# Optimization experiments

Measured on AMD Instinct MI355X. Metric: run time of the kernel, lower is better.

## Reference

```python
import jax, jax.numpy as jnp
import numpy as np

SIGMA = 1e-4          # flow-matching sigma (init kwarg)
OT_EPS = 0.01         # entropic regularization for the batched OT solve
OT_ITERS = 100        # Sinkhorn iterations


def _sinkhorn_log(M, eps, iters):
    """Log-domain Sinkhorn with uniform marginals. M: [B,N,N] cost (max-normalized).
    Returns log coupling log(pi): [B,N,N]. GPU-native batched replacement for the
    per-sample pot.emd network-simplex solve in the original."""
    B, N, _ = M.shape
    loga = -jnp.log(jnp.asarray(N, M.dtype))  # uniform marginal log prob
    f = jnp.zeros((B, N), M.dtype)
    g = jnp.zeros((B, N), M.dtype)

    def body(carry, _):
        f, g = carry
        g = eps * (loga - jax.scipy.special.logsumexp((f[:, :, None] - M) / eps, axis=1))
        f = eps * (loga - jax.scipy.special.logsumexp((g[:, None, :] - M) / eps, axis=2))
        return (f, g), None

    (f, g), _ = jax.lax.scan(body, (f, g), None, length=iters)
    return (f[:, :, None] + g[:, None, :] - M) / eps


def setup_inputs() -> dict:
    key = jax.random.key(0)
    ks = jax.random.split(key, 8)
    B, N, F, H = 512, 150, 3, 512
    x = jax.random.normal(ks[0], (B, N, F), jnp.float32)
    mask = jnp.ones((B, N, 1), jnp.float32)
    t = jax.random.uniform(ks[1], (B,), jnp.float32)
    x0_noise = jax.random.normal(ks[2], (B, N, F), jnp.float32)
    eps_noise = jax.random.normal(ks[3], (B, N, F), jnp.float32)
    W1 = 0.05 * jax.random.normal(ks[4], (F + 1, H), jnp.float32)
    b1 = jnp.zeros((H,), jnp.float32)
    W2 = 0.05 * jax.random.normal(ks[5], (H, F), jnp.float32)
    b2 = jnp.zeros((F,), jnp.float32)
    return {"x": x, "mask": mask, "t": t, "x0_noise": x0_noise,
            "eps_noise": eps_noise, "W1": W1, "b1": b1, "W2": W2, "b2": b2}


def reference(x, mask, t, x0_noise, eps_noise, W1, b1, W2, b2):
    B, N, F = x.shape
    x0, x1 = x0_noise, x                        # noise source / data target

    # squared pairwise distances, per-batch max-normalized (as in the torch code)
    M = jnp.sum((x0[:, :, None, :] - x1[:, None, :, :]) ** 2, axis=-1)  # [B,N,N]
    M = M / jnp.max(M, axis=(1, 2), keepdims=True)
    M = jax.lax.stop_gradient(M)                # original detaches M before emd

    logpi = _sinkhorn_log(M, OT_EPS, OT_ITERS)  # [B,N,N] log OT coupling

    # Sample N i.i.d. (i, j) pairs per batch from the flattened coupling.
    # Row marginal of pi is uniform -> i ~ Uniform(N), j ~ pi[i, :] / (1/N).
    key = jax.random.key(42)
    ki, kj = jax.random.split(key)
    i = jax.random.randint(ki, (B, N), 0, N)                       # [B,N]
    rows = jnp.take_along_axis(logpi, i[:, :, None], axis=1)       # [B,N,N]
    j = jax.random.categorical(kj, rows, axis=-1)                  # [B,N]

    x0s = jnp.take_along_axis(x0, i[:, :, None], axis=1)           # [B,N,F]
    x1s = jnp.take_along_axis(x1, j[:, :, None], axis=1)           # [B,N,F]
    mask_ot = jnp.take_along_axis(mask, j[:, :, None], axis=1)     # [B,N,1]

    tb = t[:, None, None]                                          # [B,1,1]
    mu_t = x0s * tb + x1s * (1.0 - tb)
    y = mu_t + SIGMA * eps_noise
    ut = (x0s - x1s) * mask_ot

    # stand-in flow network: per-particle MLP on [y, t]
    h = jnp.concatenate([y, jnp.broadcast_to(tb, (B, N, 1))], axis=-1)  # [B,N,F+1]
    h = jax.nn.gelu(h @ W1 + b1)
    vt = (h @ W2 + b2) * mask_ot

    return jnp.mean((vt - ut) ** 2)
```

## Files before the change

### kernel.cpp

```cpp
#include <hip/hip_runtime.h>
#include <cstdint>

#define B_ 512
#define N_ 150
#define NT 640
#define PPS 152
#define C1f 144.26950408889634f
#define LN2f 0.69314718055994531f
#define SIGMAf 1.0e-4f
#define INV_N (1.0f/150.0f)

#define EXP2R(x) __builtin_amdgcn_exp2f(x)
#define LOG2R(x) __builtin_amdgcn_logf(x)

#define DPPF(v, c) __int_as_float(__builtin_amdgcn_update_dpp( \
    __float_as_int(v), __float_as_int(v), (c), 0xF, 0xF, false))
#define RED4_ADD(v)  { v = v + DPPF(v, 0xB1); v = v + DPPF(v, 0x4E); }

#define REP10(X) X(0) X(1) X(2) X(3) X(4) X(5) X(6) X(7) X(8) X(9)

__host__ __device__ __forceinline__ void tf2x32(uint32_t k0, uint32_t k1,
                                                uint32_t x0, uint32_t x1,
                                                uint32_t& o0, uint32_t& o1) {
  uint32_t ks2 = k0 ^ k1 ^ 0x1BD11BDAu;
  x0 += k0; x1 += k1;
#define TFR(r) { x0 += x1; x1 = (x1 << r) | (x1 >> (32 - r)); x1 ^= x0; }
  TFR(13) TFR(15) TFR(26) TFR(6)
  x0 += k1;  x1 += ks2 + 1u;
  TFR(17) TFR(29) TFR(16) TFR(24)
  x0 += ks2; x1 += k0 + 2u;
  TFR(13) TFR(15) TFR(26) TFR(6)
  x0 += k0;  x1 += k1 + 3u;
  TFR(17) TFR(29) TFR(16) TFR(24)
  x0 += k1;  x1 += ks2 + 4u;
  TFR(13) TFR(15) TFR(26) TFR(6)
  x0 += ks2; x1 += k0 + 5u;
#undef TFR
  o0 = x0; o1 = x1;
}

__device__ __forceinline__ uint32_t jax_bits(uint32_t k0, uint32_t k1, uint32_t p) {
  uint32_t a, b; tf2x32(k0, k1, 0u, p, a, b);
  return a ^ b;
}

__global__ __launch_bounds__(NT, 5) void cfm_ot_kernel(
    const float* __restrict__ x1g, const float* __restrict__ x0g,
    float* __restrict__ pp)
{
  __shared__ float x1L[480], x0L[480];
  __shared__ __align__(16) float colp[16 * 164];
  __shared__ float rowq[160 * 11];
  __shared__ __align__(16) float vhat[160];
  __shared__ float uhat[160];
  __shared__ float red[16];
  float4* colp4 = (float4*)colp;
  float4* vhat4 = (float4*)vhat;

  const int b    = blockIdx.x;
  const int tid  = threadIdx.x;
  const int lane = tid & 63;
  const int wid  = tid >> 6;
  const int rg   = tid / 40;
  const int cg   = tid - rg * 40;
  const int q    = tid & 3;
  const int cgq  = cg >> 2;
  const int rbase = rg * 10;
  const int cbase = cg * 4;

  if (tid < 480) {
    x1L[tid] = (tid < 450) ? x1g[b * 450 + tid] : 0.f;
    x0L[tid] = (tid < 450) ? x0g[b * 450 + tid] : 0.f;
  }
  __syncthreads();

  float4 kt0, kt1, kt2, kt3, kt4, kt5, kt6, kt7, kt8, kt9;
  float lmax = 0.f;
  {
    const float c0 = x1L[cbase * 3 + 0], c1 = x1L[cbase * 3 + 1], c2 = x1L[cbase * 3 + 2];
    const float d0 = x1L[cbase * 3 + 3], d1 = x1L[cbase * 3 + 4], d2 = x1L[cbase * 3 + 5];
    const float e0 = x1L[cbase * 3 + 6], e1 = x1L[cbase * 3 + 7], e2 = x1L[cbase * 3 + 8];
    const float f0 = x1L[cbase * 3 + 9], f1 = x1L[cbase * 3 + 10], f2 = x1L[cbase * 3 + 11];
#define DIST(r) { \
    const int row = rbase + r; \
    const float rx = x0L[row * 3 + 0], ry = x0L[row * 3 + 1], rz = x0L[row * 3 + 2]; \
    float dx, dy, dz, d; \
    dx = rx - c0; dy = ry - c1; dz = rz - c2; \
    d = fmaf(dz, dz, fmaf(dy, dy, dx * dx)); \
    kt##r.x = (row < N_ && cbase + 0 < N_) ? d : 0.f; \
    dx = rx - d0; dy = ry - d1; dz = rz - d2; \
    d = fmaf(dz, dz, fmaf(dy, dy, dx * dx)); \
    kt##r.y = (row < N_ && cbase + 1 < N_) ? d : 0.f; \
    dx = rx - e0; dy = ry - e1; dz = rz - e2; \
    d = fmaf(dz, dz, fmaf(dy, dy, dx * dx)); \
    kt##r.z = (row < N_ && cbase + 2 < N_) ? d : 0.f; \
    dx = rx - f0; dy = ry - f1; dz = rz - f2; \
    d = fmaf(dz, dz, fmaf(dy, dy, dx * dx)); \
    kt##r.w = (row < N_ && cbase + 3 < N_) ? d : 0.f; \
    lmax = fmaxf(lmax, fmaxf(fmaxf(kt##r.x, kt##r.y), fmaxf(kt##r.z, kt##r.w))); }
    REP10(DIST)
#undef DIST
  }
  #pragma unroll
  for (int off = 1; off < 64; off <<= 1) lmax = fmaxf(lmax, __shfl_xor(lmax, off));
  if (lane == 0) red[wid] = lmax;
  if (tid < 160) uhat[tid] = 1.0f;
  __syncthreads();
  if (tid == 0) {
    float m = red[0];
    #pragma unroll
    for (int w = 1; w < 10; ++w) m = fmaxf(m, red[w]);
    red[15] = -C1f / m;
  }
  __syncthreads();
  const float nsc = red[15];

#define TOK(r) { \
    const int row = rbase + r; \
    kt##r.x = (row < N_ && cbase + 0 < N_) ? EXP2R(nsc * kt##r.x) : 0.f; \
    kt##r.y = (row < N_ && cbase + 1 < N_) ? EXP2R(nsc * kt##r.y) : 0.f; \
    kt##r.z = (row < N_ && cbase + 2 < N_) ? EXP2R(nsc * kt##r.z) : 0.f; \
    kt##r.w = (row < N_ && cbase + 3 < N_) ? EXP2R(nsc * kt##r.w) : 0.f; }
  REP10(TOK)
#undef TOK

  for (int it = 0; it < 100; ++it) {
    {
      float4 p4 = make_float4(0.f, 0.f, 0.f, 0.f);
#define COLA(r) { \
      const float ur = uhat[rbase + r]; \
      p4.x = fmaf(kt##r.x, ur, p4.x); \
      p4.y = fmaf(kt##r.y, ur, p4.y); \
      p4.z = fmaf(kt##r.z, ur, p4.z); \
      p4.w = fmaf(kt##r.w, ur, p4.w); }
      REP10(COLA)
#undef COLA
      colp4[rg * 41 + cg] = p4;
    }
    __syncthreads();
    if (tid < 160) {
      float s = 0.f;
      #pragma unroll
      for (int k = 0; k < 16; ++k) s += colp[k * 164 + tid];
      vhat[tid] = __builtin_amdgcn_rcpf(fmaxf(s, 1e-37f)) * INV_N;
    }
    __syncthreads();
    {
      const float4 vv = vhat4[cg];
#define ROWB(r) { \
      float rp = kt##r.x * vv.x; \
      rp = fmaf(kt##r.y, vv.y, rp); \
      rp = fmaf(kt##r.z, vv.z, rp); \
      rp = fmaf(kt##r.w, vv.w, rp); \
      RED4_ADD(rp) \
      if (q == 0) rowq[(rbase + r) * 11 + cgq] = rp; }
      REP10(ROWB)
#undef ROWB
    }
    __syncthreads();
    if (tid < 160) {
      float s = 0.f;
      #pragma unroll
      for (int u = 0; u < 10; ++u) s += rowq[tid * 11 + u];
      uhat[tid] = __builtin_amdgcn_rcpf(fmaxf(s, 1e-37f)) * INV_N;
    }
    __syncthreads();
  }

  if (tid < N_) pp[b * PPS + tid] = LOG2R(vhat[tid]);
  if (tid == 0) pp[b * PPS + 150] = nsc;
}

__global__ __launch_bounds__(NT) void cfm_sample_kernel(
    const float* __restrict__ x1g, const float* __restrict__ maskg,
    const float* __restrict__ tg, const float* __restrict__ x0g,
    const float* __restrict__ epsg,
    const float* __restrict__ W1, const float* __restrict__ b1,
    const float* __restrict__ W2, const float* __restrict__ b2,
    const float* __restrict__ pp, float* __restrict__ partials,
    uint32_t kj0, uint32_t kj1, uint32_t k1r0, uint32_t k1r1,
    uint32_t k2r0, uint32_t k2r1)
{
  __shared__ float x1L[450], x0L[450], psiS[152], mskS[152];
  __shared__ float yu[150 * 9];
  __shared__ float red[16];
  __shared__ int   iselS[152];

  const int b    = blockIdx.x;
  const int tid  = threadIdx.x;
  const int lane = tid & 63;
  const int wid  = tid >> 6;

  if (tid < 450) {
    x1L[tid] = x1g[b * 450 + tid];
    x0L[tid] = x0g[b * 450 + tid];
  }
  if (tid < N_) {
    psiS[tid] = pp[b * PPS + tid];
    mskS[tid] = maskg[b * 150 + tid];
    const uint32_t p = (uint32_t)(b * N_ + tid);
    const uint32_t hb = jax_bits(k1r0, k1r1, p);
    const uint32_t lb = jax_bits(k2r0, k2r1, p);
    iselS[tid] = (int)(((hb % 150u) * 46u + (lb % 150u)) % 150u);
  }
  const float nsc = pp[b * PPS + 150];
  const float tb  = tg[b];
  __syncthreads();

  for (int n = wid; n < N_; n += 10) {
    const uint32_t p = (uint32_t)(b * N_ + n);
    const int isel = iselS[n];
    const float xi0 = x0L[isel * 3 + 0], xi1 = x0L[isel * 3 + 1], xi2 = x0L[isel * 3 + 2];

    float best = -1e30f; int bestk = 0x7fffffff;
    #pragma unroll
    for (int c2 = 0; c2 < 3; ++c2) {
      const int k = lane + 64 * c2;
      if (k < N_) {
        const uint32_t bits = jax_bits(kj0, kj1, p * 150u + (uint32_t)k);
        float u = __uint_as_float((bits >> 9) | 0x3F800000u) - 1.0f;
        u = fmaxf(u, 1.17549435e-38f);
        const float nlu = -LN2f * LOG2R(u);
        const float g = -LN2f * LOG2R(nlu);
        const float dx = xi0 - x1L[k * 3 + 0];
        const float dy = xi1 - x1L[k * 3 + 1];
        const float dz = xi2 - x1L[k * 3 + 2];
        const float d2 = fmaf(dz, dz, fmaf(dy, dy, dx * dx));
        const float val = fmaf(psiS[k] + nsc * d2, LN2f, g);
        if (val > best || (val == best && k < bestk)) { best = val; bestk = k; }
      }
    }
    #pragma unroll
    for (int off = 1; off < 64; off <<= 1) {
      const float ov = __shfl_xor(best, off);
      const int   ok = __shfl_xor(bestk, off);
      if (ov > best || (ov == best && ok < bestk)) { best = ov; bestk = ok; }
    }
    if (lane == 0) {
      const int j = bestk;
      const float mot = mskS[j];
      const float q0 = x1L[j * 3 + 0], q1 = x1L[j * 3 + 1], q2 = x1L[j * 3 + 2];
      const float omt = 1.f - tb;
      yu[n * 9 + 0] = xi0 * tb + q0 * omt + SIGMAf * epsg[b * 450 + n * 3 + 0];
      yu[n * 9 + 1] = xi1 * tb + q1 * omt + SIGMAf * epsg[b * 450 + n * 3 + 1];
      yu[n * 9 + 2] = xi2 * tb + q2 * omt + SIGMAf * epsg[b * 450 + n * 3 + 2];
      yu[n * 9 + 3] = (xi0 - q0) * mot;
      yu[n * 9 + 4] = (xi1 - q1) * mot;
      yu[n * 9 + 5] = (xi2 - q2) * mot;
      yu[n * 9 + 6] = mot;
    }
  }
  __syncthreads();

  float loss = 0.f;
  if (wid < 3) {
    const int n = wid * 64 + lane;
    if (n < N_) {
      const float y0 = yu[n * 9 + 0], y1 = yu[n * 9 + 1], y2 = yu[n * 9 + 2];
      const float u0 = yu[n * 9 + 3], u1 = yu[n * 9 + 4], u2 = yu[n * 9 + 5];
      const float mot = yu[n * 9 + 6];
      float a0 = 0.f, a1 = 0.f, a2 = 0.f;
      #pragma unroll 4
      for (int hd = 0; hd < 512; ++hd) {
        float z = b1[hd];
        z = fmaf(y0, W1[hd],        z);
        z = fmaf(y1, W1[512 + hd],  z);
        z = fmaf(y2, W1[1024 + hd], z);
        z = fmaf(tb, W1[1536 + hd], z);
        const float zc = fmaf(0.044715f * z, z * z, z);
        const float e2 = EXP2R(-2.3022082062161855f * zc);
        const float ge = z * __builtin_amdgcn_rcpf(1.f + e2);
        a0 = fmaf(ge, W2[hd * 3 + 0], a0);
        a1 = fmaf(ge, W2[hd * 3 + 1], a1);
        a2 = fmaf(ge, W2[hd * 3 + 2], a2);
      }
      const float v0 = (a0 + b2[0]) * mot;
      const float v1 = (a1 + b2[1]) * mot;
      const float v2 = (a2 + b2[2]) * mot;
      const float d0 = v0 - u0, d1 = v1 - u1, d2 = v2 - u2;
      loss = fmaf(d2, d2, fmaf(d1, d1, d0 * d0));
    }
    #pragma unroll
    for (int off = 1; off < 64; off <<= 1) loss += __shfl_xor(loss, off);
    if (lane == 0) red[wid] = loss;
  }
  __syncthreads();
  if (tid == 0) partials[b] = red[0] + red[1] + red[2];
}

__global__ void cfm_reduce_kernel(const float* __restrict__ partials,
                                  float* __restrict__ out) {
  const int tid = threadIdx.x;
  float s = 0.f;
  #pragma unroll
  for (int q = 0; q < 8; ++q) s += partials[tid + 64 * q];
  #pragma unroll
  for (int off = 1; off < 64; off <<= 1) s += __shfl_xor(s, off);
  if (tid == 0) out[0] = s * (1.0f / 230400.0f);
}

extern "C" void kernel_launch(void* const* d_in, const int* in_sizes, int n_in,
                              void* d_out, int out_size, void* d_ws, size_t ws_size,
                              hipStream_t stream) {
  (void)in_sizes; (void)n_in; (void)out_size; (void)ws_size;
  const float* x    = (const float*)d_in[0];
  const float* mask = (const float*)d_in[1];
  const float* t    = (const float*)d_in[2];
  const float* x0n  = (const float*)d_in[3];
  const float* epsn = (const float*)d_in[4];
  const float* W1   = (const float*)d_in[5];
  const float* b1   = (const float*)d_in[6];
  const float* W2   = (const float*)d_in[7];
  const float* b2   = (const float*)d_in[8];
  float* out = (float*)d_out;

  float* pp       = (float*)d_ws;
  float* partials = pp + B_ * PPS;

  uint32_t ki0, ki1, kj0, kj1, k1r0, k1r1, k2r0, k2r1;
  tf2x32(0u, 42u, 0u, 0u, ki0, ki1);
  tf2x32(0u, 42u, 0u, 1u, kj0, kj1);
  tf2x32(ki0, ki1, 0u, 0u, k1r0, k1r1);
  tf2x32(ki0, ki1, 0u, 1u, k2r0, k2r1);

  cfm_ot_kernel<<<B_, NT, 0, stream>>>(x, x0n, pp);
  cfm_sample_kernel<<<B_, NT, 0, stream>>>(x, mask, t, x0n, epsn, W1, b1, W2, b2,
                                           pp, partials,
                                           kj0, kj1, k1r0, k1r1, k2r0, k2r1);
  cfm_reduce_kernel<<<1, 64, 0, stream>>>(partials, out);
}
```

Before: 271.2 us.

## Fuse Sinkhorn and sampling kernels; store kernel twice for reduction-free updates

Merges the OT Sinkhorn kernel and the sampling/MLP kernel into one launch, dropping the global round trip of the log potentials. Each thread now keeps both a column-major and a row-major copy of its share of the Gibbs kernel (4 threads per row/column), so every half-iteration finishes with an in-quad DPP reduction instead of a shared-memory partial write plus a second reduction pass. This cuts the barriers per Sinkhorn iteration from four to two. The cost is roughly twice the register footprint for the kernel copies while keeping launch_bounds(640,5), plus the extra shared memory of the fused sampling stage, which may reduce occupancy or cause spills.

```diff
diff --git a/kernel.cpp b/kernel.cpp
--- a/kernel.cpp
+++ b/kernel.cpp
@@ -4,7 +4,6 @@
 #define B_ 512
 #define N_ 150
 #define NT 640
-#define PPS 152
 #define C1f 144.26950408889634f
 #define LN2f 0.69314718055994531f
 #define SIGMAf 1.0e-4f
@@ -45,66 +44,79 @@
 }
 
 __global__ __launch_bounds__(NT, 5) void cfm_ot_kernel(
-    const float* __restrict__ x1g, const float* __restrict__ x0g,
-    float* __restrict__ pp)
+    const float* __restrict__ x1g, const float* __restrict__ maskg,
+    const float* __restrict__ tg, const float* __restrict__ x0g,
+    const float* __restrict__ epsg,
+    const float* __restrict__ W1, const float* __restrict__ b1,
+    const float* __restrict__ W2, const float* __restrict__ b2,
+    float* __restrict__ partials,
+    uint32_t kj0, uint32_t kj1, uint32_t k1r0, uint32_t k1r1,
+    uint32_t k2r0, uint32_t k2r1)
 {
   __shared__ float x1L[480], x0L[480];
-  __shared__ __align__(16) float colp[16 * 164];
-  __shared__ float rowq[160 * 11];
   __shared__ __align__(16) float vhat[160];
-  __shared__ float uhat[160];
+  __shared__ __align__(16) float uhat[160];
   __shared__ float red[16];
-  float4* colp4 = (float4*)colp;
+  __shared__ float psiS[152], mskS[152];
+  __shared__ float yu[150 * 9];
+  __shared__ int   iselS[152];
   float4* vhat4 = (float4*)vhat;
+  float4* uhat4 = (float4*)uhat;
 
   const int b    = blockIdx.x;
   const int tid  = threadIdx.x;
   const int lane = tid & 63;
   const int wid  = tid >> 6;
-  const int rg   = tid / 40;
-  const int cg   = tid - rg * 40;
-  const int q    = tid & 3;
-  const int cgq  = cg >> 2;
-  const int rbase = rg * 10;
-  const int cbase = cg * 4;
+  const int jA   = tid >> 2;
+  const int qA   = tid & 3;
+  const int rcb  = 40 * qA;
+  const bool act = (jA < N_);
 
   if (tid < 480) {
     x1L[tid] = (tid < 450) ? x1g[b * 450 + tid] : 0.f;
     x0L[tid] = (tid < 450) ? x0g[b * 450 + tid] : 0.f;
   }
-  __syncthreads();
-
-  float4 kt0, kt1, kt2, kt3, kt4, kt5, kt6, kt7, kt8, kt9;
+  if (tid < 160) uhat[tid] = 1.0f;
+  __syncthreads();
+
+  float4 ca0, ca1, ca2, ca3, ca4, ca5, ca6, ca7, ca8, ca9;
+  float4 rb0, rb1, rb2, rb3, rb4, rb5, rb6, rb7, rb8, rb9;
   float lmax = 0.f;
   {
-    const float c0 = x1L[cbase * 3 + 0], c1 = x1L[cbase * 3 + 1], c2 = x1L[cbase * 3 + 2];
-    const float d0 = x1L[cbase * 3 + 3], d1 = x1L[cbase * 3 + 4], d2 = x1L[cbase * 3 + 5];
-    const float e0 = x1L[cbase * 3 + 6], e1 = x1L[cbase * 3 + 7], e2 = x1L[cbase * 3 + 8];
-    const float f0 = x1L[cbase * 3 + 9], f1 = x1L[cbase * 3 + 10], f2 = x1L[cbase * 3 + 11];
-#define DIST(r) { \
-    const int row = rbase + r; \
-    const float rx = x0L[row * 3 + 0], ry = x0L[row * 3 + 1], rz = x0L[row * 3 + 2]; \
-    float dx, dy, dz, d; \
-    dx = rx - c0; dy = ry - c1; dz = rz - c2; \
-    d = fmaf(dz, dz, fmaf(dy, dy, dx * dx)); \
-    kt##r.x = (row < N_ && cbase + 0 < N_) ? d : 0.f; \
-    dx = rx - d0; dy = ry - d1; dz = rz - d2; \
-    d = fmaf(dz, dz, fmaf(dy, dy, dx * dx)); \
-    kt##r.y = (row < N_ && cbase + 1 < N_) ? d : 0.f; \
-    dx = rx - e0; dy = ry - e1; dz = rz - e2; \
-    d = fmaf(dz, dz, fmaf(dy, dy, dx * dx)); \
-    kt##r.z = (row < N_ && cbase + 2 < N_) ? d : 0.f; \
-    dx = rx - f0; dy = ry - f1; dz = rz - f2; \
-    d = fmaf(dz, dz, fmaf(dy, dy, dx * dx)); \
-    kt##r.w = (row < N_ && cbase + 3 < N_) ? d : 0.f; \
-    lmax = fmaxf(lmax, fmaxf(fmaxf(kt##r.x, kt##r.y), fmaxf(kt##r.z, kt##r.w))); }
-    REP10(DIST)
-#undef DIST
+    const float cx = x1L[jA * 3 + 0], cy = x1L[jA * 3 + 1], cz = x1L[jA * 3 + 2];
+#define DCA(k) { \
+    float tmp[4]; \
+    _Pragma("unroll") \
+    for (int c = 0; c < 4; ++c) { \
+      const int row = rcb + 4 * k + c; \
+      const float dx = x0L[row * 3 + 0] - cx; \
+      const float dy = x0L[row * 3 + 1] - cy; \
+      const float dz = x0L[row * 3 + 2] - cz; \
+      float d = fmaf(dz, dz, fmaf(dy, dy, dx * dx)); \
+      d = (act && row < N_) ? d : 0.f; \
+      lmax = fmaxf(lmax, d); \
+      tmp[c] = d; } \
+    ca##k = make_float4(tmp[0], tmp[1], tmp[2], tmp[3]); }
+    REP10(DCA)
+#undef DCA
+    const float rx = x0L[jA * 3 + 0], ry = x0L[jA * 3 + 1], rz = x0L[jA * 3 + 2];
+#define DRB(k) { \
+    float tmp[4]; \
+    _Pragma("unroll") \
+    for (int c = 0; c < 4; ++c) { \
+      const int cc = rcb + 4 * k + c; \
+      const float dx = rx - x1L[cc * 3 + 0]; \
+      const float dy = ry - x1L[cc * 3 + 1]; \
+      const float dz = rz - x1L[cc * 3 + 2]; \
+      const float d = fmaf(dz, dz, fmaf(dy, dy, dx * dx)); \
+      tmp[c] = (act && cc < N_) ? d : 0.f; } \
+    rb##k = make_float4(tmp[0], tmp[1], tmp[2], tmp[3]); }
+    REP10(DRB)
+#undef DRB
   }
   #pragma unroll
   for (int off = 1; off < 64; off <<= 1) lmax = fmaxf(lmax, __shfl_xor(lmax, off));
   if (lane == 0) red[wid] = lmax;
-  if (tid < 160) uhat[tid] = 1.0f;
   __syncthreads();
   if (tid == 0) {
     float m = red[0];
@@ -115,96 +127,65 @@
   __syncthreads();
   const float nsc = red[15];
 
-#define TOK(r) { \
-    const int row = rbase + r; \
-    kt##r.x = (row < N_ && cbase + 0 < N_) ? EXP2R(nsc * kt##r.x) : 0.f; \
-    kt##r.y = (row < N_ && cbase + 1 < N_) ? EXP2R(nsc * kt##r.y) : 0.f; \
-    kt##r.z = (row < N_ && cbase + 2 < N_) ? EXP2R(nsc * kt##r.z) : 0.f; \
-    kt##r.w = (row < N_ && cbase + 3 < N_) ? EXP2R(nsc * kt##r.w) : 0.f; }
+#define TOK(k) { \
+    const int rA0 = rcb + 4 * k; \
+    ca##k.x = (act && rA0 + 0 < N_) ? EXP2R(nsc * ca##k.x) : 0.f; \
+    ca##k.y = (act && rA0 + 1 < N_) ? EXP2R(nsc * ca##k.y) : 0.f; \
+    ca##k.z = (act && rA0 + 2 < N_) ? EXP2R(nsc * ca##k.z) : 0.f; \
+    ca##k.w = (act && rA0 + 3 < N_) ? EXP2R(nsc * ca##k.w) : 0.f; \
+    rb##k.x = (act && rA0 + 0 < N_) ? EXP2R(nsc * rb##k.x) : 0.f; \
+    rb##k.y = (act && rA0 + 1 < N_) ? EXP2R(nsc * rb##k.y) : 0.f; \
+    rb##k.z = (act && rA0 + 2 < N_) ? EXP2R(nsc * rb##k.z) : 0.f; \
+    rb##k.w = (act && rA0 + 3 < N_) ? EXP2R(nsc * rb##k.w) : 0.f; }
   REP10(TOK)
 #undef TOK
 
+  const int ubase = 10 * qA;
+
   for (int it = 0; it < 100; ++it) {
     {
-      float4 p4 = make_float4(0.f, 0.f, 0.f, 0.f);
-#define COLA(r) { \
-      const float ur = uhat[rbase + r]; \
-      p4.x = fmaf(kt##r.x, ur, p4.x); \
-      p4.y = fmaf(kt##r.y, ur, p4.y); \
-      p4.z = fmaf(kt##r.z, ur, p4.z); \
-      p4.w = fmaf(kt##r.w, ur, p4.w); }
+      float s0 = 0.f, s1 = 0.f, s2 = 0.f, s3 = 0.f;
+#define COLA(k) { \
+      const float4 u4 = uhat4[ubase + k]; \
+      s0 = fmaf(ca##k.x, u4.x, s0); \
+      s1 = fmaf(ca##k.y, u4.y, s1); \
+      s2 = fmaf(ca##k.z, u4.z, s2); \
+      s3 = fmaf(ca##k.w, u4.w, s3); }
       REP10(COLA)
 #undef COLA
-      colp4[rg * 41 + cg] = p4;
-    }
-    __syncthreads();
-    if (tid < 160) {
-      float s = 0.f;
-      #pragma unroll
-      for (int k = 0; k < 16; ++k) s += colp[k * 164 + tid];
-      vhat[tid] = __builtin_amdgcn_rcpf(fmaxf(s, 1e-37f)) * INV_N;
+      float s = (s0 + s1) + (s2 + s3);
+      RED4_ADD(s)
+      const float vh = __builtin_amdgcn_rcpf(fmaxf(s, 1e-37f)) * INV_N;
+      if (qA == 0) vhat[jA] = vh;
     }
     __syncthreads();
     {
-      const float4 vv = vhat4[cg];
-#define ROWB(r) { \
-      float rp = kt##r.x * vv.x; \
-      rp = fmaf(kt##r.y, vv.y, rp); \
-      rp = fmaf(kt##r.z, vv.z, rp); \
-      rp = fmaf(kt##r.w, vv.w, rp); \
-      RED4_ADD(rp) \
-      if (q == 0) rowq[(rbase + r) * 11 + cgq] = rp; }
+      float t0 = 0.f, t1 = 0.f, t2 = 0.f, t3 = 0.f;
+#define ROWB(k) { \
+      const float4 v4 = vhat4[ubase + k]; \
+      t0 = fmaf(rb##k.x, v4.x, t0); \
+      t1 = fmaf(rb##k.y, v4.y, t1); \
+      t2 = fmaf(rb##k.z, v4.z, t2); \
+      t3 = fmaf(rb##k.w, v4.w, t3); }
       REP10(ROWB)
 #undef ROWB
+      float t = (t0 + t1) + (t2 + t3);
+      RED4_ADD(t)
+      const float uh = __builtin_amdgcn_rcpf(fmaxf(t, 1e-37f)) * INV_N;
+      if (qA == 0) uhat[jA] = uh;
     }
     __syncthreads();
-    if (tid < 160) {
-      float s = 0.f;
-      #pragma unroll
-      for (int u = 0; u < 10; ++u) s += rowq[tid * 11 + u];
-      uhat[tid] = __builtin_amdgcn_rcpf(fmaxf(s, 1e-37f)) * INV_N;
-    }
-    __syncthreads();
-  }
-
-  if (tid < N_) pp[b * PPS + tid] = LOG2R(vhat[tid]);
-  if (tid == 0) pp[b * PPS + 150] = nsc;
-}
-
-__global__ __launch_bounds__(NT) void cfm_sample_kernel(
-    const float* __restrict__ x1g, const float* __restrict__ maskg,
-    const float* __restrict__ tg, const float* __restrict__ x0g,
-    const float* __restrict__ epsg,
-    const float* __restrict__ W1, const float* __restrict__ b1,
-    const float* __restrict__ W2, const float* __restrict__ b2,
-    const float* __restrict__ pp, float* __restrict__ partials,
-    uint32_t kj0, uint32_t kj1, uint32_t k1r0, uint32_t k1r1,
-    uint32_t k2r0, uint32_t k2r1)
-{
-  __shared__ float x1L[450], x0L[450], psiS[152], mskS[152];
-  __shared__ float yu[150 * 9];
-  __shared__ float red[16];
-  __shared__ int   iselS[152];
-
-  const int b    = blockIdx.x;
-  const int tid  = threadIdx.x;
-  const int lane = tid & 63;
-  const int wid  = tid >> 6;
-
-  if (tid < 450) {
-    x1L[tid] = x1g[b * 450 + tid];
-    x0L[tid] = x0g[b * 450 + tid];
-  }
+  }
+
   if (tid < N_) {
-    psiS[tid] = pp[b * PPS + tid];
+    psiS[tid] = LOG2R(vhat[tid]);
     mskS[tid] = maskg[b * 150 + tid];
     const uint32_t p = (uint32_t)(b * N_ + tid);
     const uint32_t hb = jax_bits(k1r0, k1r1, p);
     const uint32_t lb = jax_bits(k2r0, k2r1, p);
     iselS[tid] = (int)(((hb % 150u) * 46u + (lb % 150u)) % 150u);
   }
-  const float nsc = pp[b * PPS + 150];
-  const float tb  = tg[b];
+  const float tb = tg[b];
   __syncthreads();
 
   for (int n = wid; n < N_; n += 10) {
@@ -313,9 +294,7 @@
   const float* W2   = (const float*)d_in[7];
   const float* b2   = (const float*)d_in[8];
   float* out = (float*)d_out;
-
-  float* pp       = (float*)d_ws;
-  float* partials = pp + B_ * PPS;
+  float* partials = (float*)d_ws;
 
   uint32_t ki0, ki1, kj0, kj1, k1r0, k1r1, k2r0, k2r1;
   tf2x32(0u, 42u, 0u, 0u, ki0, ki1);
@@ -323,9 +302,8 @@
   tf2x32(ki0, ki1, 0u, 0u, k1r0, k1r1);
   tf2x32(ki0, ki1, 0u, 1u, k2r0, k2r1);
 
-  cfm_ot_kernel<<<B_, NT, 0, stream>>>(x, x0n, pp);
-  cfm_sample_kernel<<<B_, NT, 0, stream>>>(x, mask, t, x0n, epsn, W1, b1, W2, b2,
-                                           pp, partials,
-                                           kj0, kj1, k1r0, k1r1, k2r0, k2r1);
+  cfm_ot_kernel<<<B_, NT, 0, stream>>>(x, mask, t, x0n, epsn, W1, b1, W2, b2,
+                                       partials,
+                                       kj0, kj1, k1r0, k1r1, k2r0, k2r1);
   cfm_reduce_kernel<<<1, 64, 0, stream>>>(partials, out);
 }
```

Result: slower. 392.1 us (+44.6%).

## Process two batch elements per block in Sinkhorn kernel to amortize barriers

Applied to the files above, without the earlier changes.

Each block of the OT kernel now runs Sinkhorn for two batch elements at once, holding both kernel matrices in registers and sharing each __syncthreads across both problems. Grid size halves and launch bounds drop from 5 to 3 blocks per SM to allow double the register footprint. The goal is to cut barrier and latency overhead per problem and add ILP, but lower occupancy and only 256 blocks may underfill the GPU's compute units.

```diff
diff --git a/kernel.cpp b/kernel.cpp
--- a/kernel.cpp
+++ b/kernel.cpp
@@ -44,20 +44,23 @@
   return a ^ b;
 }
 
-__global__ __launch_bounds__(NT, 5) void cfm_ot_kernel(
+__global__ __launch_bounds__(NT, 3) void cfm_ot_kernel(
     const float* __restrict__ x1g, const float* __restrict__ x0g,
     float* __restrict__ pp)
 {
-  __shared__ float x1L[480], x0L[480];
-  __shared__ __align__(16) float colp[16 * 164];
-  __shared__ float rowq[160 * 11];
-  __shared__ __align__(16) float vhat[160];
-  __shared__ float uhat[160];
-  __shared__ float red[16];
-  float4* colp4 = (float4*)colp;
-  float4* vhat4 = (float4*)vhat;
-
-  const int b    = blockIdx.x;
+  __shared__ float x1A[480], x0A[480], x1B[480], x0B[480];
+  __shared__ __align__(16) float colpA[16 * 164], colpB[16 * 164];
+  __shared__ float rowqA[160 * 11], rowqB[160 * 11];
+  __shared__ __align__(16) float vhatA[160], vhatB[160];
+  __shared__ float uhatA[160], uhatB[160];
+  __shared__ float red[32];
+  float4* colpA4 = (float4*)colpA;
+  float4* colpB4 = (float4*)colpB;
+  float4* vhatA4 = (float4*)vhatA;
+  float4* vhatB4 = (float4*)vhatB;
+
+  const int b0   = 2 * blockIdx.x;
+  const int b1   = b0 + 1;
   const int tid  = threadIdx.x;
   const int lane = tid & 63;
   const int wid  = tid >> 6;
@@ -69,91 +72,142 @@
   const int cbase = cg * 4;
 
   if (tid < 480) {
-    x1L[tid] = (tid < 450) ? x1g[b * 450 + tid] : 0.f;
-    x0L[tid] = (tid < 450) ? x0g[b * 450 + tid] : 0.f;
-  }
-  __syncthreads();
-
-  float4 kt0, kt1, kt2, kt3, kt4, kt5, kt6, kt7, kt8, kt9;
-  float lmax = 0.f;
-  {
-    const float c0 = x1L[cbase * 3 + 0], c1 = x1L[cbase * 3 + 1], c2 = x1L[cbase * 3 + 2];
-    const float d0 = x1L[cbase * 3 + 3], d1 = x1L[cbase * 3 + 4], d2 = x1L[cbase * 3 + 5];
-    const float e0 = x1L[cbase * 3 + 6], e1 = x1L[cbase * 3 + 7], e2 = x1L[cbase * 3 + 8];
-    const float f0 = x1L[cbase * 3 + 9], f1 = x1L[cbase * 3 + 10], f2 = x1L[cbase * 3 + 11];
-#define DIST(r) { \
-    const int row = rbase + r; \
-    const float rx = x0L[row * 3 + 0], ry = x0L[row * 3 + 1], rz = x0L[row * 3 + 2]; \
-    float dx, dy, dz, d; \
-    dx = rx - c0; dy = ry - c1; dz = rz - c2; \
-    d = fmaf(dz, dz, fmaf(dy, dy, dx * dx)); \
-    kt##r.x = (row < N_ && cbase + 0 < N_) ? d : 0.f; \
-    dx = rx - d0; dy = ry - d1; dz = rz - d2; \
-    d = fmaf(dz, dz, fmaf(dy, dy, dx * dx)); \
-    kt##r.y = (row < N_ && cbase + 1 < N_) ? d : 0.f; \
-    dx = rx - e0; dy = ry - e1; dz = rz - e2; \
-    d = fmaf(dz, dz, fmaf(dy, dy, dx * dx)); \
-    kt##r.z = (row < N_ && cbase + 2 < N_) ? d : 0.f; \
-    dx = rx - f0; dy = ry - f1; dz = rz - f2; \
-    d = fmaf(dz, dz, fmaf(dy, dy, dx * dx)); \
-    kt##r.w = (row < N_ && cbase + 3 < N_) ? d : 0.f; \
-    lmax = fmaxf(lmax, fmaxf(fmaxf(kt##r.x, kt##r.y), fmaxf(kt##r.z, kt##r.w))); }
-    REP10(DIST)
-#undef DIST
-  }
+    x1A[tid] = (tid < 450) ? x1g[b0 * 450 + tid] : 0.f;
+    x0A[tid] = (tid < 450) ? x0g[b0 * 450 + tid] : 0.f;
+    x1B[tid] = (tid < 450) ? x1g[b1 * 450 + tid] : 0.f;
+    x0B[tid] = (tid < 450) ? x0g[b1 * 450 + tid] : 0.f;
+  }
+  if (tid < 160) { uhatA[tid] = 1.0f; uhatB[tid] = 1.0f; }
+  __syncthreads();
+
+  float4 ktA0, ktA1, ktA2, ktA3, ktA4, ktA5, ktA6, ktA7, ktA8, ktA9;
+  float4 ktB0, ktB1, ktB2, ktB3, ktB4, ktB5, ktB6, ktB7, ktB8, ktB9;
+  float lmaxA = 0.f, lmaxB = 0.f;
+#define DISTS(S) { \
+    const float c0 = x1##S[cbase * 3 + 0], c1 = x1##S[cbase * 3 + 1], c2 = x1##S[cbase * 3 + 2]; \
+    const float d0 = x1##S[cbase * 3 + 3], d1 = x1##S[cbase * 3 + 4], d2 = x1##S[cbase * 3 + 5]; \
+    const float e0 = x1##S[cbase * 3 + 6], e1 = x1##S[cbase * 3 + 7], e2 = x1##S[cbase * 3 + 8]; \
+    const float f0 = x1##S[cbase * 3 + 9], f1 = x1##S[cbase * 3 + 10], f2 = x1##S[cbase * 3 + 11]; \
+    _Pragma("unroll") \
+    for (int r = 0; r < 10; ++r) { \
+      const int row = rbase + r; \
+      const float rx = x0##S[row * 3 + 0], ry = x0##S[row * 3 + 1], rz = x0##S[row * 3 + 2]; \
+      float dx, dy, dz, d; float t0_, t1_, t2_, t3_; \
+      dx = rx - c0; dy = ry - c1; dz = rz - c2; \
+      d = fmaf(dz, dz, fmaf(dy, dy, dx * dx)); \
+      t0_ = (row < N_ && cbase + 0 < N_) ? d : 0.f; \
+      dx = rx - d0; dy = ry - d1; dz = rz - d2; \
+      d = fmaf(dz, dz, fmaf(dy, dy, dx * dx)); \
+      t1_ = (row < N_ && cbase + 1 < N_) ? d : 0.f; \
+      dx = rx - e0; dy = ry - e1; dz = rz - e2; \
+      d = fmaf(dz, dz, fmaf(dy, dy, dx * dx)); \
+      t2_ = (row < N_ && cbase + 2 < N_) ? d : 0.f; \
+      dx = rx - f0; dy = ry - f1; dz = rz - f2; \
+      d = fmaf(dz, dz, fmaf(dy, dy, dx * dx)); \
+      t3_ = (row < N_ && cbase + 3 < N_) ? d : 0.f; \
+      lmax##S = fmaxf(lmax##S, fmaxf(fmaxf(t0_, t1_), fmaxf(t2_, t3_))); \
+      switch (r) { \
+        case 0: kt##S##0 = make_float4(t0_, t1_, t2_, t3_); break; \
+        case 1: kt##S##1 = make_float4(t0_, t1_, t2_, t3_); break; \
+        case 2: kt##S##2 = make_float4(t0_, t1_, t2_, t3_); break; \
+        case 3: kt##S##3 = make_float4(t0_, t1_, t2_, t3_); break; \
+        case 4: kt##S##4 = make_float4(t0_, t1_, t2_, t3_); break; \
+        case 5: kt##S##5 = make_float4(t0_, t1_, t2_, t3_); break; \
+        case 6: kt##S##6 = make_float4(t0_, t1_, t2_, t3_); break; \
+        case 7: kt##S##7 = make_float4(t0_, t1_, t2_, t3_); break; \
+        case 8: kt##S##8 = make_float4(t0_, t1_, t2_, t3_); break; \
+        case 9: kt##S##9 = make_float4(t0_, t1_, t2_, t3_); break; \
+      } } }
+  DISTS(A)
+  DISTS(B)
+#undef DISTS
   #pragma unroll
-  for (int off = 1; off < 64; off <<= 1) lmax = fmaxf(lmax, __shfl_xor(lmax, off));
-  if (lane == 0) red[wid] = lmax;
-  if (tid < 160) uhat[tid] = 1.0f;
+  for (int off = 1; off < 64; off <<= 1) {
+    lmaxA = fmaxf(lmaxA, __shfl_xor(lmaxA, off));
+    lmaxB = fmaxf(lmaxB, __shfl_xor(lmaxB, off));
+  }
+  if (lane == 0) { red[wid] = lmaxA; red[10 + wid] = lmaxB; }
   __syncthreads();
   if (tid == 0) {
-    float m = red[0];
+    float mA = red[0], mB = red[10];
     #pragma unroll
-    for (int w = 1; w < 10; ++w) m = fmaxf(m, red[w]);
-    red[15] = -C1f / m;
-  }
-  __syncthreads();
-  const float nsc = red[15];
-
-#define TOK(r) { \
-    const int row = rbase + r; \
-    kt##r.x = (row < N_ && cbase + 0 < N_) ? EXP2R(nsc * kt##r.x) : 0.f; \
-    kt##r.y = (row < N_ && cbase + 1 < N_) ? EXP2R(nsc * kt##r.y) : 0.f; \
-    kt##r.z = (row < N_ && cbase + 2 < N_) ? EXP2R(nsc * kt##r.z) : 0.f; \
-    kt##r.w = (row < N_ && cbase + 3 < N_) ? EXP2R(nsc * kt##r.w) : 0.f; }
-  REP10(TOK)
+    for (int w = 1; w < 10; ++w) { mA = fmaxf(mA, red[w]); mB = fmaxf(mB, red[10 + w]); }
+    red[30] = -C1f / mA;
+    red[31] = -C1f / mB;
+  }
+  __syncthreads();
+  const float nscA = red[30];
+  const float nscB = red[31];
+
+#define TOK(S, k) { \
+    const int rA0 = rbase + k; (void)rA0; \
+    kt##S##k.x = (rbase + k < N_ + 0 || true) ? kt##S##k.x : 0.f; }
 #undef TOK
+#define TOKR(S, k) { \
+    const int row = rbase + k; \
+    kt##S##k.x = (row < N_ && cbase + 0 < N_) ? EXP2R(nsc##S * kt##S##k.x) : 0.f; \
+    kt##S##k.y = (row < N_ && cbase + 1 < N_) ? EXP2R(nsc##S * kt##S##k.y) : 0.f; \
+    kt##S##k.z = (row < N_ && cbase + 2 < N_) ? EXP2R(nsc##S * kt##S##k.z) : 0.f; \
+    kt##S##k.w = (row < N_ && cbase + 3 < N_) ? EXP2R(nsc##S * kt##S##k.w) : 0.f; }
+#define TOKA(k) TOKR(A, k)
+#define TOKB(k) TOKR(B, k)
+  REP10(TOKA)
+  REP10(TOKB)
+#undef TOKA
+#undef TOKB
+#undef TOKR
 
   for (int it = 0; it < 100; ++it) {
     {
-      float4 p4 = make_float4(0.f, 0.f, 0.f, 0.f);
-#define COLA(r) { \
-      const float ur = uhat[rbase + r]; \
-      p4.x = fmaf(kt##r.x, ur, p4.x); \
-      p4.y = fmaf(kt##r.y, ur, p4.y); \
-      p4.z = fmaf(kt##r.z, ur, p4.z); \
-      p4.w = fmaf(kt##r.w, ur, p4.w); }
+      float4 pA = make_float4(0.f, 0.f, 0.f, 0.f);
+      float4 pB = make_float4(0.f, 0.f, 0.f, 0.f);
+#define COLA(k) { \
+      const float urA = uhatA[rbase + k]; \
+      const float urB = uhatB[rbase + k]; \
+      pA.x = fmaf(ktA##k.x, urA, pA.x); \
+      pA.y = fmaf(ktA##k.y, urA, pA.y); \
+      pA.z = fmaf(ktA##k.z, urA, pA.z); \
+      pA.w = fmaf(ktA##k.w, urA, pA.w); \
+      pB.x = fmaf(ktB##k.x, urB, pB.x); \
+      pB.y = fmaf(ktB##k.y, urB, pB.y); \
+      pB.z = fmaf(ktB##k.z, urB, pB.z); \
+      pB.w = fmaf(ktB##k.w, urB, pB.w); }
       REP10(COLA)
 #undef COLA
-      colp4[rg * 41 + cg] = p4;
+      colpA4[rg * 41 + cg] = pA;
+      colpB4[rg * 41 + cg] = pB;
     }
     __syncthreads();
     if (tid < 160) {
       float s = 0.f;
       #pragma unroll
-      for (int k = 0; k < 16; ++k) s += colp[k * 164 + tid];
-      vhat[tid] = __builtin_amdgcn_rcpf(fmaxf(s, 1e-37f)) * INV_N;
+      for (int k = 0; k < 16; ++k) s += colpA[k * 164 + tid];
+      vhatA[tid] = __builtin_amdgcn_rcpf(fmaxf(s, 1e-37f)) * INV_N;
+    } else if (tid >= 320 && tid < 480) {
+      const int c = tid - 320;
+      float s = 0.f;
+      #pragma unroll
+      for (int k = 0; k < 16; ++k) s += colpB[k * 164 + c];
+      vhatB[c] = __builtin_amdgcn_rcpf(fmaxf(s, 1e-37f)) * INV_N;
     }
     __syncthreads();
     {
-      const float4 vv = vhat4[cg];
-#define ROWB(r) { \
-      float rp = kt##r.x * vv.x; \
-      rp = fmaf(kt##r.y, vv.y, rp); \
-      rp = fmaf(kt##r.z, vv.z, rp); \
-      rp = fmaf(kt##r.w, vv.w, rp); \
-      RED4_ADD(rp) \
-      if (q == 0) rowq[(rbase + r) * 11 + cgq] = rp; }
+      const float4 vA = vhatA4[cg];
+      const float4 vB = vhatB4[cg];
+#define ROWB(k) { \
+      float rpA = ktA##k.x * vA.x; \
+      rpA = fmaf(ktA##k.y, vA.y, rpA); \
+      rpA = fmaf(ktA##k.z, vA.z, rpA); \
+      rpA = fmaf(ktA##k.w, vA.w, rpA); \
+      float rpB = ktB##k.x * vB.x; \
+      rpB = fmaf(ktB##k.y, vB.y, rpB); \
+      rpB = fmaf(ktB##k.z, vB.z, rpB); \
+      rpB = fmaf(ktB##k.w, vB.w, rpB); \
+      RED4_ADD(rpA) \
+      RED4_ADD(rpB) \
+      if (q == 0) { \
+        rowqA[(rbase + k) * 11 + cgq] = rpA; \
+        rowqB[(rbase + k) * 11 + cgq] = rpB; } }
       REP10(ROWB)
 #undef ROWB
     }
@@ -161,14 +215,26 @@
     if (tid < 160) {
       float s = 0.f;
       #pragma unroll
-      for (int u = 0; u < 10; ++u) s += rowq[tid * 11 + u];
-      uhat[tid] = __builtin_amdgcn_rcpf(fmaxf(s, 1e-37f)) * INV_N;
+      for (int u = 0; u < 10; ++u) s += rowqA[tid * 11 + u];
+      uhatA[tid] = __builtin_amdgcn_rcpf(fmaxf(s, 1e-37f)) * INV_N;
+    } else if (tid >= 320 && tid < 480) {
+      const int c = tid - 320;
+      float s = 0.f;
+      #pragma unroll
+      for (int u = 0; u < 10; ++u) s += rowqB[c * 11 + u];
+      uhatB[c] = __builtin_amdgcn_rcpf(fmaxf(s, 1e-37f)) * INV_N;
     }
     __syncthreads();
   }
 
-  if (tid < N_) pp[b * PPS + tid] = LOG2R(vhat[tid]);
-  if (tid == 0) pp[b * PPS + 150] = nsc;
+  if (tid < N_) {
+    pp[b0 * PPS + tid] = LOG2R(vhatA[tid]);
+    pp[b1 * PPS + tid] = LOG2R(vhatB[tid]);
+  }
+  if (tid == 0) {
+    pp[b0 * PPS + 150] = nscA;
+    pp[b1 * PPS + 150] = nscB;
+  }
 }
 
 __global__ __launch_bounds__(NT) void cfm_sample_kernel(
@@ -323,7 +389,7 @@
   tf2x32(ki0, ki1, 0u, 0u, k1r0, k1r1);
   tf2x32(ki0, ki1, 0u, 1u, k2r0, k2r1);
 
-  cfm_ot_kernel<<<B_, NT, 0, stream>>>(x, x0n, pp);
+  cfm_ot_kernel<<<B_ / 2, NT, 0, stream>>>(x, x0n, pp);
   cfm_sample_kernel<<<B_, NT, 0, stream>>>(x, mask, t, x0n, epsn, W1, b1, W2, b2,
                                            pp, partials,
                                            kj0, kj1, k1r0, k1r1, k2r0, k2r1);
```

Result: slower. 288.3 us (+6.3%).
